# Kernel optimization log

Measured on AMD Instinct MI355X. Metric: run time of the kernel, lower is better.

The kernel has to match this reference:

```python
import jax, jax.numpy as jnp
import numpy as np

ALIGNED_H, ALIGNED_W = 7, 7          # module init args
AH, AW = ALIGNED_H + 1, ALIGNED_W + 1  # RoIAlignFunction sampling grid (8x8)


def setup_inputs() -> dict:
    key = jax.random.key(0)
    k1, k2, k3, k4 = jax.random.split(key, 4)
    B, C, H, W = 4, 256, 200, 200
    N = 1024
    spatial_scale = jnp.float32(1.0 / 16.0)
    img = H / (1.0 / 16.0)  # 3200 px image-space extent
    features = jax.random.normal(k1, (B, C, H, W), dtype=jnp.float32)
    bidx = jax.random.randint(k2, (N,), 0, B).astype(jnp.float32)
    xy1 = jax.random.uniform(k3, (N, 2), minval=0.0, maxval=img - 64.0)
    wh = jax.random.uniform(k4, (N, 2), minval=16.0, maxval=512.0)
    xy2 = jnp.minimum(xy1 + wh, img - 1.0)
    rois = jnp.concatenate(
        [bidx[:, None], xy1[:, 0:1], xy1[:, 1:2], xy2[:, 0:1], xy2[:, 1:2]], axis=1
    ).astype(jnp.float32)
    return {"features": features, "rois": rois, "spatial_scale": spatial_scale}


def _roi_align(features, rois, spatial_scale):
    B, C, H, W = features.shape
    b = rois[:, 0].astype(jnp.int32)
    x1 = rois[:, 1] * spatial_scale
    y1 = rois[:, 2] * spatial_scale
    x2 = rois[:, 3] * spatial_scale
    y2 = rois[:, 4] * spatial_scale
    bin_h = jnp.maximum(y2 - y1 + 1.0, 0.0) / (AH - 1)   # [N]
    bin_w = jnp.maximum(x2 - x1 + 1.0, 0.0) / (AW - 1)
    ph = jnp.arange(AH, dtype=features.dtype)
    pw = jnp.arange(AW, dtype=features.dtype)
    h = y1[:, None] + ph * bin_h[:, None]                 # [N, AH] sample rows
    w = x1[:, None] + pw * bin_w[:, None]                 # [N, AW] sample cols
    hs_f = jnp.minimum(jnp.floor(h), H - 2.0)             # clip as in CUDA kernel
    ws_f = jnp.minimum(jnp.floor(w), W - 2.0)
    hr = h - hs_f                                         # bilinear ratios
    wr = w - ws_f
    hi = jnp.clip(hs_f, 0.0, None).astype(jnp.int32)      # safe gather indices
    wi = jnp.clip(ws_f, 0.0, None).astype(jnp.int32)
    valid = ((h >= 0) & (h < H))[:, :, None] & ((w >= 0) & (w < W))[:, None, :]
    bb = b[:, None, None]
    Hg = hi[:, :, None]
    Wg = wi[:, None, :]

    def g(dh, dw):
        # advanced-index gather -> [N, AH, AW, C]
        return features[bb, :, Hg + dh, Wg + dw]

    hr_ = hr[:, :, None, None]
    wr_ = wr[:, None, :, None]
    val = (g(0, 0) * (1 - hr_) * (1 - wr_)
           + g(0, 1) * (1 - hr_) * wr_
           + g(1, 0) * hr_ * (1 - wr_)
           + g(1, 1) * hr_ * wr_)
    val = jnp.where(valid[..., None], val, 0.0)
    return jnp.transpose(val, (0, 3, 1, 2))               # [N, C, AH, AW]


def reference(features, rois, spatial_scale):
    x = _roi_align(features, rois, spatial_scale)
    # avg_pool2d(kernel_size=2, stride=1): 8x8 -> 7x7
    return (x[:, :, :-1, :-1] + x[:, :, :-1, 1:]
            + x[:, :, 1:, :-1] + x[:, :, 1:, 1:]) * 0.25
```

## Files before the change

### kernel.cpp

```cpp
#include <hip/hip_runtime.h>

#define BATCH   4
#define CH      256
#define FH      200
#define FW      200
#define NROI    1024
#define PLANE   (FH * FW)
#define POOL    7
#define SAMP    8
#define CGROUPS 8
#define CH_PER_WAVE 8

__global__ __launch_bounds__(256) void roialign_avg_kernel(
    const float* __restrict__ feat,
    const float* __restrict__ rois,
    const float* __restrict__ scale_p,
    float* __restrict__ out)
{
    const int n    = blockIdx.x;
    const int g    = blockIdx.y;
    const int tid  = threadIdx.x;
    const int wave = tid >> 6;
    const int lane = tid & 63;
    const int ph   = lane >> 3;
    const int pw   = lane & 7;

    const float scale = scale_p[0];
    const int   b  = (int)rois[n * 5 + 0];
    const float x1 = rois[n * 5 + 1] * scale;
    const float y1 = rois[n * 5 + 2] * scale;
    const float x2 = rois[n * 5 + 3] * scale;
    const float y2 = rois[n * 5 + 4] * scale;

    const float bin_h = fmaxf(y2 - y1 + 1.0f, 0.0f) / 7.0f;
    const float bin_w = fmaxf(x2 - x1 + 1.0f, 0.0f) / 7.0f;

    const float h    = y1 + (float)ph * bin_h;
    const float w    = x1 + (float)pw * bin_w;
    const float hs_f = fminf(floorf(h), (float)(FH - 2));
    const float ws_f = fminf(floorf(w), (float)(FW - 2));
    const float hr   = h - hs_f;
    const float wr   = w - ws_f;
    const int   hi   = (int)fmaxf(hs_f, 0.0f);
    const int   wi   = (int)fmaxf(ws_f, 0.0f);
    const bool  valid = (h >= 0.0f) && (h < (float)FH) &&
                        (w >= 0.0f) && (w < (float)FW);
    const float m = valid ? 0.25f : 0.0f;

    const float w00 = (1.0f - hr) * (1.0f - wr) * m;
    const float w01 = (1.0f - hr) * wr * m;
    const float w10 = hr * (1.0f - wr) * m;
    const float w11 = hr * wr * m;

    const int c0 = g * (4 * CH_PER_WAVE) + wave * CH_PER_WAVE;

    const float* p = feat + ((size_t)(b * CH + c0)) * PLANE
                          + (size_t)(hi * FW + wi);
    float* outp = out + ((size_t)n * CH + c0) * (POOL * POOL) + ph * POOL + pw;

    const bool do_store = (ph < POOL) && (pw < POOL);

#pragma unroll
    for (int dc = 0; dc < CH_PER_WAVE; ++dc) {
        const float g00 = p[0];
        const float g01 = p[1];
        const float g10 = p[FW];
        const float g11 = p[FW + 1];
        float v = g00 * w00 + g01 * w01 + g10 * w10 + g11 * w11;

        float s1 = v + __shfl_down(v, 1, 64);
        float s2 = s1 + __shfl_down(s1, 8, 64);

        if (do_store) __builtin_nontemporal_store(s2, outp);

        p    += PLANE;
        outp += POOL * POOL;
    }
}

extern "C" void kernel_launch(void* const* d_in, const int* in_sizes, int n_in,
                              void* d_out, int out_size, void* d_ws, size_t ws_size,
                              hipStream_t stream) {
    const float* feat    = (const float*)d_in[0];
    const float* rois    = (const float*)d_in[1];
    const float* scale_p = (const float*)d_in[2];
    float*       out     = (float*)d_out;
    (void)in_sizes; (void)n_in; (void)out_size; (void)d_ws; (void)ws_size;

    dim3 grid(NROI, CGROUPS);
    dim3 block(256);
    hipLaunchKernelGGL(roialign_avg_kernel, grid, block, 0, stream,
                       feat, rois, scale_p, out);
}
```

Measured before the change: 276.1 us.

## Stage full feature plane in LDS and sweep all RoIs per channel

Reorganizes the grid so each block owns one (batch, channel) plane, copies the whole 200x200 plane into shared memory with vectorized loads, then has each wave iterate over RoIs and sample bilinearly from LDS. This replaces scattered global gathers, which reread feature data per RoI, with a single coalesced read per plane. In exchange each block scans all RoIs and discards those from other batches, occupancy drops to one 1024-thread block per CU, and the full-plane load is not overlapped with compute.

After: 320.0 us. +15.9%, slower.

```diff
diff --git a/kernel.cpp b/kernel.cpp
--- a/kernel.cpp
+++ b/kernel.cpp
@@ -1,80 +1,85 @@
 #include <hip/hip_runtime.h>
 
-#define BATCH   4
-#define CH      256
-#define FH      200
-#define FW      200
-#define NROI    1024
-#define PLANE   (FH * FW)
-#define POOL    7
-#define SAMP    8
-#define CGROUPS 8
-#define CH_PER_WAVE 8
+#define BATCH 4
+#define CH    256
+#define FH    200
+#define FW    200
+#define NROI  1024
+#define PLANE (FH * FW)
+#define POOL  7
+#define NWAVE 16
 
-__global__ __launch_bounds__(256) void roialign_avg_kernel(
+__global__ __launch_bounds__(1024, 1) void roialign_lds_kernel(
     const float* __restrict__ feat,
     const float* __restrict__ rois,
     const float* __restrict__ scale_p,
     float* __restrict__ out)
 {
-    const int n    = blockIdx.x;
-    const int g    = blockIdx.y;
-    const int tid  = threadIdx.x;
+    __shared__ float splane[PLANE];
+
+    const int c   = blockIdx.x;
+    const int b   = blockIdx.y;
+    const int tid = threadIdx.x;
+
+    {
+        const float4* __restrict__ src =
+            (const float4*)(feat + ((size_t)b * CH + c) * PLANE);
+        float4* dst = (float4*)splane;
+        for (int i = tid; i < PLANE / 4; i += 1024)
+            dst[i] = src[i];
+    }
+    __syncthreads();
+
+    const float scale = scale_p[0];
     const int wave = tid >> 6;
     const int lane = tid & 63;
     const int ph   = lane >> 3;
     const int pw   = lane & 7;
-
-    const float scale = scale_p[0];
-    const int   b  = (int)rois[n * 5 + 0];
-    const float x1 = rois[n * 5 + 1] * scale;
-    const float y1 = rois[n * 5 + 2] * scale;
-    const float x2 = rois[n * 5 + 3] * scale;
-    const float y2 = rois[n * 5 + 4] * scale;
-
-    const float bin_h = fmaxf(y2 - y1 + 1.0f, 0.0f) / 7.0f;
-    const float bin_w = fmaxf(x2 - x1 + 1.0f, 0.0f) / 7.0f;
-
-    const float h    = y1 + (float)ph * bin_h;
-    const float w    = x1 + (float)pw * bin_w;
-    const float hs_f = fminf(floorf(h), (float)(FH - 2));
-    const float ws_f = fminf(floorf(w), (float)(FW - 2));
-    const float hr   = h - hs_f;
-    const float wr   = w - ws_f;
-    const int   hi   = (int)fmaxf(hs_f, 0.0f);
-    const int   wi   = (int)fmaxf(ws_f, 0.0f);
-    const bool  valid = (h >= 0.0f) && (h < (float)FH) &&
-                        (w >= 0.0f) && (w < (float)FW);
-    const float m = valid ? 0.25f : 0.0f;
-
-    const float w00 = (1.0f - hr) * (1.0f - wr) * m;
-    const float w01 = (1.0f - hr) * wr * m;
-    const float w10 = hr * (1.0f - wr) * m;
-    const float w11 = hr * wr * m;
-
-    const int c0 = g * (4 * CH_PER_WAVE) + wave * CH_PER_WAVE;
-
-    const float* p = feat + ((size_t)(b * CH + c0)) * PLANE
-                          + (size_t)(hi * FW + wi);
-    float* outp = out + ((size_t)n * CH + c0) * (POOL * POOL) + ph * POOL + pw;
-
     const bool do_store = (ph < POOL) && (pw < POOL);
 
-#pragma unroll
-    for (int dc = 0; dc < CH_PER_WAVE; ++dc) {
-        const float g00 = p[0];
-        const float g01 = p[1];
-        const float g10 = p[FW];
-        const float g11 = p[FW + 1];
-        float v = g00 * w00 + g01 * w01 + g10 * w10 + g11 * w11;
+    for (int n = wave; n < NROI; n += NWAVE) {
+        const int rb = (int)rois[n * 5 + 0];
+        if (rb != b) continue;
+
+        const float x1 = rois[n * 5 + 1] * scale;
+        const float y1 = rois[n * 5 + 2] * scale;
+        const float x2 = rois[n * 5 + 3] * scale;
+        const float y2 = rois[n * 5 + 4] * scale;
+
+        const float bin_h = fmaxf(y2 - y1 + 1.0f, 0.0f) * (1.0f / 7.0f);
+        const float bin_w = fmaxf(x2 - x1 + 1.0f, 0.0f) * (1.0f / 7.0f);
+
+        const float h    = y1 + (float)ph * bin_h;
+        const float w    = x1 + (float)pw * bin_w;
+        const float hs_f = fminf(floorf(h), (float)(FH - 2));
+        const float ws_f = fminf(floorf(w), (float)(FW - 2));
+        const float hr   = h - hs_f;
+        const float wr   = w - ws_f;
+        const int   hi   = (int)fmaxf(hs_f, 0.0f);
+        const int   wi   = (int)fmaxf(ws_f, 0.0f);
+        const bool  valid = (h >= 0.0f) && (h < (float)FH) &&
+                            (w >= 0.0f) && (w < (float)FW);
+        const float m = valid ? 0.25f : 0.0f;
+
+        const float w00 = (1.0f - hr) * (1.0f - wr) * m;
+        const float w01 = (1.0f - hr) * wr * m;
+        const float w10 = hr * (1.0f - wr) * m;
+        const float w11 = hr * wr * m;
+
+        const int off = hi * FW + wi;
+        const float g00 = splane[off];
+        const float g01 = splane[off + 1];
+        const float g10 = splane[off + FW];
+        const float g11 = splane[off + FW + 1];
+
+        float v  = g00 * w00 + g01 * w01 + g10 * w10 + g11 * w11;
 
         float s1 = v + __shfl_down(v, 1, 64);
         float s2 = s1 + __shfl_down(s1, 8, 64);
 
-        if (do_store) __builtin_nontemporal_store(s2, outp);
-
-        p    += PLANE;
-        outp += POOL * POOL;
+        if (do_store)
+            __builtin_nontemporal_store(
+                s2, out + ((size_t)n * CH + c) * (POOL * POOL) + ph * POOL + pw);
     }
 }
 
@@ -87,8 +92,8 @@
     float*       out     = (float*)d_out;
     (void)in_sizes; (void)n_in; (void)out_size; (void)d_ws; (void)ws_size;
 
-    dim3 grid(NROI, CGROUPS);
-    dim3 block(256);
-    hipLaunchKernelGGL(roialign_avg_kernel, grid, block, 0, stream,
+    dim3 grid(CH, BATCH);
+    dim3 block(1024);
+    hipLaunchKernelGGL(roialign_lds_kernel, grid, block, 0, stream,
                        feat, rois, scale_p, out);
 }
```
